# Optimization experiments

Hardware: AMD Instinct MI355X
Metric: run time of the kernel (lower is better)

## Reference

```python
import jax, jax.numpy as jnp
import numpy as np
from itertools import combinations

WAY = 5
TSS = 3  # temporal_set_size


def setup_inputs() -> dict:
    key = jax.random.key(0)
    k1, k2, k3 = jax.random.split(key, 3)
    n_support, n_queries, seq_len, D = 25, 400, 8, 2048
    d_out = D // 2
    support_set = jax.random.normal(k1, (n_support, seq_len, D), dtype=jnp.float32)
    queries = jax.random.normal(k2, (n_queries, seq_len, D), dtype=jnp.float32)
    support_labels = jnp.arange(n_support, dtype=jnp.int64) % WAY  # shot=5 per class
    W = jax.random.normal(k3, (d_out, TSS * D), dtype=jnp.float32) * 0.02
    b = jnp.zeros((d_out,), dtype=jnp.float32)
    return {"support_set": support_set, "support_labels": support_labels,
            "queries": queries, "W": W, "b": b}


def reference(support_set, support_labels, queries, W, b):
    # Dropout is identity at inference; omitted for determinism.
    n_s, seq_len, D = support_set.shape
    n_q = queries.shape[0]
    tup = jnp.asarray(list(combinations(range(seq_len), TSS)))  # [Tn, 3]
    Tn = tup.shape[0]
    # gather frame tuples and flatten: [N, Tn, 3*D]
    s = support_set[:, tup, :].reshape(n_s, Tn, TSS * D)
    q = queries[:, tup, :].reshape(n_q, Tn, TSS * D)
    # Linear + ReLU embedding
    qe = jax.nn.relu(q.reshape(n_q * Tn, TSS * D) @ W.T + b)          # [Q*Tn, d2]
    se = jax.nn.relu(s.reshape(n_s * Tn, TSS * D) @ W.T + b)
    se = se.reshape(n_s, Tn, -1)
    # group support by class (labels are static ints; shot per class is equal)
    order = jnp.argsort(support_labels, stable=True)                  # sorted by label
    cls_se = se[order.reshape(WAY, -1)].reshape(WAY, -1, se.shape[-1])  # [way, shot*Tn, d2]
    # pairwise Euclidean distances per class: ||q||^2 + ||s||^2 - 2 q.s
    q2 = jnp.sum(qe * qe, axis=-1)                                    # [Q*Tn]
    s2 = jnp.sum(cls_se * cls_se, axis=-1)                            # [way, shot*Tn]
    dots = jnp.einsum('qd,csd->cqs', qe, cls_se)                      # [way, Q*Tn, shot*Tn]
    dist = jnp.sqrt(jnp.maximum(q2[None, :, None] + s2[:, None, :] - 2.0 * dots, 0.0))
    min_dist = dist.min(axis=2).reshape(WAY, n_q, Tn)                 # min over class supports
    logits = -min_dist.mean(axis=2).T                                 # [n_q, way]
    return logits
```

## Files before the change

### kernel.cpp

```cpp
#include <hip/hip_runtime.h>
#include <math.h>

#define NSUP 25
#define NQ   400
#define SL   8
#define DIM  2048
#define DOUT 1024
#define WAY  5
#define TN   56
#define SHOT 5
#define QT   (NQ*TN)
#define STC  (SHOT*TN)
#define NFS  (NSUP*SL)
#define NFQ  (NQ*SL)
#define MF   (NFS+NFQ)
#define MFP  3584
#define PN   (3*DOUT)
#define NSE  1400
#define NSEP 1408

typedef __attribute__((ext_vector_type(8))) short short8;
typedef __attribute__((ext_vector_type(8))) int   int8v;
typedef __attribute__((ext_vector_type(4))) float f32x4;

#define GLOAD_LDS(g, l) __builtin_amdgcn_global_load_lds( \
    (const __attribute__((address_space(1))) unsigned*)(g), \
    (__attribute__((address_space(3))) unsigned*)(l), 16, 0, 0)

__device__ __forceinline__ unsigned short f2bf(float x) {
  unsigned u = __float_as_uint(x);
  u += 0x7fff + ((u >> 16) & 1);
  return (unsigned short)(u >> 16);
}
__device__ __forceinline__ float bf2f(unsigned short h) {
  return __uint_as_float(((unsigned)h) << 16);
}
__device__ __forceinline__ unsigned pk4_fp8(float a, float b, float c, float d) {
  unsigned p = __builtin_amdgcn_cvt_pk_fp8_f32(a, b, 0, false);
  p = __builtin_amdgcn_cvt_pk_fp8_f32(c, d, p, true);
  return p;
}
__device__ __forceinline__ float f8deq(unsigned b) {
  unsigned e = (b >> 3) & 15, m = b & 7;
  return e ? ldexpf((float)(8 + m), (int)e - 10) : ldexpf((float)m, -9);
}

__device__ __constant__ unsigned short TUP[TN] = {
  0x210,0x310,0x410,0x510,0x610,0x710,
  0x320,0x420,0x520,0x620,0x720,
  0x430,0x530,0x630,0x730,
  0x540,0x640,0x740,
  0x650,0x750,
  0x760,
  0x321,0x421,0x521,0x621,0x721,
  0x431,0x531,0x631,0x731,
  0x541,0x641,0x741,
  0x651,0x751,
  0x761,
  0x432,0x532,0x632,0x732,
  0x542,0x642,0x742,
  0x652,0x752,
  0x762,
  0x543,0x643,0x743,
  0x653,0x753,
  0x763,
  0x654,0x754,
  0x764,
  0x765
};

__global__ __launch_bounds__(256) void prep(
    const float* __restrict__ sup, const float* __restrict__ qry,
    const float* __restrict__ W,
    unsigned char* __restrict__ A8, unsigned char* __restrict__ W8,
    unsigned char* __restrict__ se8, float* __restrict__ s2,
    unsigned* __restrict__ pmin)
{
  int idx = blockIdx.x * 256 + threadIdx.x;
  {
    int e = idx * 4;
    int row = e >> 11, c = e & 2047;
    float4 v = make_float4(0.f, 0.f, 0.f, 0.f);
    if (row < NFS)      v = *(const float4*)(sup + (size_t)row * DIM + c);
    else if (row < MF)  v = *(const float4*)(qry + (size_t)(row - NFS) * DIM + c);
    *(unsigned*)(A8 + e) = pk4_fp8(v.x, v.y, v.z, v.w);
  }
  if (idx < PN*DIM/4) {
    int e = idx * 4;
    int n = e >> 11, c = e & 2047;
    const float4 v = *(const float4*)(W + (size_t)(n & 1023) * (3*DIM) + (n >> 10) * DIM + c);
    *(unsigned*)(W8 + e) = pk4_fp8(v.x*64.f, v.y*64.f, v.z*64.f, v.w*64.f);
  }
  if (idx < WAY * QT) pmin[idx] = 0x7F800000u;
  if (idx < (NSEP - NSE) * DOUT) se8[(size_t)NSE * DOUT + idx] = 0;
  if (idx < NSEP - NSE) s2[NSE + idx] = 0.f;
}

__device__ __forceinline__ void mfma_kloop_f8(
    const unsigned char* __restrict__ gA, const unsigned char* __restrict__ gB,
    int sa, int sb, int rowA0, int rowB0, int clampA,
    unsigned char* As, unsigned char* Bs,
    int w, int l, int nk, f32x4 acc[8][4])
{
  const int lrow = l >> 3;
  const int cswz = ((((l >> 1) & 3) ^ (lrow & 3)) * 2 + (l & 1)) * 16;
  unsigned offA[8], offB[4];
#pragma unroll
  for (int q = 0; q < 8; ++q)
    offA[q] = (unsigned)min(rowA0 + w*64 + q*8 + lrow, clampA) * sa + cswz;
#pragma unroll
  for (int q = 0; q < 4; ++q)
    offB[q] = (unsigned)(rowB0 + w*32 + q*8 + lrow) * sb + cswz;
  unsigned char* lA = As + (w*64) * 128;
  unsigned char* lB = Bs + (w*32) * 128;
  const int lane15 = l & 15, quad = l >> 4;
  const int wm = (w & 1) * 128, wn = (w >> 1) * 64;
  const int slot = (quad ^ (lane15 & 3)) * 32;

  int koff = 0;
  for (int kk = 0; kk < nk; ++kk, koff += 128) {
    __syncthreads();
#pragma unroll
    for (int q = 0; q < 8; ++q) GLOAD_LDS(gA + offA[q] + koff, lA + q*1024);
#pragma unroll
    for (int q = 0; q < 4; ++q) GLOAD_LDS(gB + offB[q] + koff, lB + q*1024);
    __syncthreads();
    int8v af[8];
#pragma unroll
    for (int i = 0; i < 8; ++i)
      af[i] = *(const int8v*)(As + (wm + i*16 + lane15)*128 + slot);
#pragma unroll
    for (int j = 0; j < 4; ++j) {
      int8v bf = *(const int8v*)(Bs + (wn + j*16 + lane15)*128 + slot);
#pragma unroll
      for (int i = 0; i < 8; ++i)
        acc[i][j] = __builtin_amdgcn_mfma_scale_f32_16x16x128_f8f6f4(
            af[i], bf, acc[i][j], 0, 0, 0, 0x7f7f7f7f, 0, 0x7f7f7f7f);
    }
  }
}

__global__ __launch_bounds__(256, 2) void gemm_embed_f8(
    const unsigned char* __restrict__ A8, const unsigned char* __restrict__ W8,
    unsigned short* __restrict__ P)
{
  __shared__ unsigned char As[256*128];
  __shared__ unsigned char Bs[128*128];
  const int bm = blockIdx.x * 256, bn = blockIdx.y * 128;
  const int tid = threadIdx.x, w = tid >> 6, l = tid & 63;
  const int lane15 = l & 15, quad = l >> 4;
  const int wm = (w & 1) * 128, wn = (w >> 1) * 64;

  f32x4 acc[8][4] = {};
  mfma_kloop_f8(A8, W8, DIM, DIM, bm, bn, MFP-1, As, Bs, w, l, DIM/128, acc);

#pragma unroll
  for (int i = 0; i < 8; ++i) {
#pragma unroll
    for (int r = 0; r < 4; ++r) {
      int row = bm + wm + i*16 + quad*4 + r;
      if (row < MF) {
#pragma unroll
        for (int j = 0; j < 4; ++j) {
          int col = bn + wn + j*16 + lane15;
          P[(size_t)row * PN + col] = f2bf(acc[i][j][r] * 0.015625f);
        }
      }
    }
  }
}

__global__ __launch_bounds__(256) void assemble_seq(
    const unsigned short* __restrict__ P, const float* __restrict__ bias,
    unsigned char* __restrict__ qe8, float* __restrict__ q2,
    unsigned char* __restrict__ se8, float* __restrict__ s2)
{
  __shared__ unsigned short sP[SL * PN];
  const int b2 = blockIdx.x, b = b2 >> 1, half = b2 & 1;
  const int tid = threadIdx.x, w = tid >> 6, l = tid & 63;

  const size_t base = (size_t)b * SL * PN;
#pragma unroll
  for (int qi = 0; qi < 12; ++qi) {
    int off = (qi * 256 + tid) * 8;
    *(short8*)&sP[off] = *(const short8*)(P + base + off);
  }
  __syncthreads();

  float4 bbv[4];
#pragma unroll
  for (int c = 0; c < 4; ++c)
    bbv[c] = *(const float4*)&bias[l*4 + c*256];

  const bool is_sup = b < NSUP;
  unsigned char* E = is_sup ? se8 : qe8;
  float* nrm = is_sup ? s2 : q2;
  int row_base;
  if (is_sup) { int cc = b % WAY, kk = b / WAY; row_base = cc * STC + kk * TN; }
  else        { row_base = (b - NSUP) * TN; }

  const int t_end = half * 28 + 28;
  for (int t = half * 28 + w; t < t_end; t += 4) {
    unsigned int tp = TUP[t];
    int f0 = tp & 15, f1 = (tp >> 4) & 15, f2 = (tp >> 8) & 15;
    int row = row_base + t;
    float ssq = 0.f;
#pragma unroll
    for (int c = 0; c < 4; ++c) {
      int o = l*4 + c*256;
      ushort4 a = *(const ushort4*)&sP[f0*PN + o];
      ushort4 bq = *(const ushort4*)&sP[f1*PN + DOUT + o];
      ushort4 d = *(const ushort4*)&sP[f2*PN + 2*DOUT + o];
      float z0 = fmaxf(bf2f(a.x) + bf2f(bq.x) + bf2f(d.x) + bbv[c].x, 0.f);
      float z1 = fmaxf(bf2f(a.y) + bf2f(bq.y) + bf2f(d.y) + bbv[c].y, 0.f);
      float z2 = fmaxf(bf2f(a.z) + bf2f(bq.z) + bf2f(d.z) + bbv[c].z, 0.f);
      float z3 = fmaxf(bf2f(a.w) + bf2f(bq.w) + bf2f(d.w) + bbv[c].w, 0.f);
      unsigned pk = pk4_fp8(z0, z1, z2, z3);
      *(unsigned*)&E[(size_t)row * DOUT + o] = pk;
      float x0 = f8deq(pk & 255),         x1 = f8deq((pk >> 8) & 255);
      float x2 = f8deq((pk >> 16) & 255), x3 = f8deq(pk >> 24);
      ssq += x0*x0 + x1*x1 + x2*x2 + x3*x3;
    }
#pragma unroll
    for (int off = 1; off < 64; off <<= 1) ssq += __shfl_xor(ssq, off, 64);
    if (l == 0) nrm[row] = ssq;
  }
}

__global__ __launch_bounds__(256, 2) void gemm_dist_f8(
    const unsigned char* __restrict__ qe8, const unsigned char* __restrict__ se8,
    const float* __restrict__ q2, const float* __restrict__ s2,
    unsigned* __restrict__ pmin)
{
  __shared__ unsigned char As[256*128];
  __shared__ unsigned char Bs[128*128];
  const int bm = blockIdx.x * 256;
  const int bn = blockIdx.y * 128;
  const int tid = threadIdx.x, w = tid >> 6, l = tid & 63;
  const int lane15 = l & 15, quad = l >> 4;
  const int wm = (w & 1) * 128, wn = (w >> 1) * 64;

  f32x4 acc[8][4] = {};
  mfma_kloop_f8(se8, qe8, DOUT, DOUT, bm, bn, NSEP-1, As, Bs, w, l, DOUT/128, acc);

  float s2v[8][4]; int clsv[8][4];
#pragma unroll
  for (int i = 0; i < 8; ++i)
#pragma unroll
    for (int r = 0; r < 4; ++r) {
      int sec = bm + wm + i*16 + quad*4 + r;
      s2v[i][r] = s2[min(sec, NSEP-1)];
      clsv[i][r] = sec / STC;
    }
#pragma unroll
  for (int i = 0; i < 8; ++i)
#pragma unroll
    for (int j = 0; j < 4; ++j)
#pragma unroll
      for (int r = 0; r < 4; ++r)
        acc[i][j][r] = fmaf(-2.f, acc[i][j][r], s2v[i][r]);

  float q2v[4];
#pragma unroll
  for (int j = 0; j < 4; ++j)
    q2v[j] = q2[bn + wn + j*16 + lane15];

  const int c_lo = (bm + wm) / STC;
  const int c_hi = min((bm + wm + 127) / STC, WAY - 1);
  for (int c = c_lo; c <= c_hi; ++c) {
#pragma unroll
    for (int j = 0; j < 4; ++j) {
      float mv = INFINITY;
#pragma unroll
      for (int i = 0; i < 8; ++i)
#pragma unroll
        for (int r = 0; r < 4; ++r)
          mv = fminf(mv, (clsv[i][r] == c) ? acc[i][j][r] : INFINITY);
      mv = fminf(mv, __shfl_xor(mv, 16, 64));
      mv = fminf(mv, __shfl_xor(mv, 32, 64));
      if (quad == 0) {
        float val = fmaxf(q2v[j] + mv, 0.f);
        atomicMin(&pmin[(size_t)c * QT + bn + wn + j*16 + lane15],
                  __float_as_uint(val));
      }
    }
  }
}

__global__ void finalize(const unsigned* __restrict__ pmin, float* __restrict__ out)
{
  int idx = blockIdx.x * blockDim.x + threadIdx.x;
  if (idx >= NQ * WAY) return;
  int i = idx / WAY, c = idx % WAY;
  float sum = 0.f;
  for (int t = 0; t < TN; ++t) {
    float v = __uint_as_float(pmin[(size_t)c * QT + i * TN + t]);
    sum += sqrtf(v);
  }
  out[i * WAY + c] = -sum * (1.f / (float)TN);
}

extern "C" void kernel_launch(void* const* d_in, const int* in_sizes, int n_in,
                              void* d_out, int out_size, void* d_ws, size_t ws_size,
                              hipStream_t stream) {
  const float* support = (const float*)d_in[0];
  const float* queries  = (const float*)d_in[2];
  const float* W        = (const float*)d_in[3];
  const float* bias     = (const float*)d_in[4];
  float* out = (float*)d_out;

  char* ws = (char*)d_ws;
  unsigned char* A8 = (unsigned char*)ws;           ws += (size_t)MFP * DIM;
  unsigned char* W8 = (unsigned char*)ws;           ws += (size_t)PN * DIM;
  unsigned short* P = (unsigned short*)ws;          ws += (size_t)MF * PN * 2;
  unsigned char* qe8 = (unsigned char*)ws;          ws += (size_t)QT * DOUT;
  unsigned char* se8 = (unsigned char*)ws;          ws += (size_t)NSEP * DOUT;
  float*         q2  = (float*)ws;                  ws += (size_t)QT * 4;
  float*         s2  = (float*)ws;                  ws += (size_t)NSEP * 4;
  unsigned*      pm  = (unsigned*)ws;

  prep<<<MFP*DIM/4/256, 256, 0, stream>>>(support, queries, W, A8, W8, se8, s2, pm);
  gemm_embed_f8<<<dim3(MFP/256, PN/128), 256, 0, stream>>>(A8, W8, P);
  assemble_seq<<<2*(NSUP + NQ), 256, 0, stream>>>(P, bias, qe8, q2, se8, s2);
  gemm_dist_f8<<<dim3(6, QT/128), 256, 0, stream>>>(qe8, se8, q2, s2, pm);
  finalize<<<(NQ*WAY + 255)/256, 256, 0, stream>>>(pm, out);
}
```

Baseline: 204.7 us.

## Rearrange LDS tile layout for MFMA fragments and swizzle dist-GEMM block order

Changes how the global-to-LDS async loads place data so each 16-row MFMA fragment is contiguous in LDS. Each lane now reads two 16-byte chunks 256 bytes apart instead of one 32-byte swizzled slot, which is meant to cut LDS bank conflicts on fragment reads. Separately, the distance GEMM launch becomes a 1D grid of 1050 blocks remapped so groups of 8 query tiles sweep all 6 support tiles together, aiming to improve L2 reuse of the query embeddings. The new mapping drops the XOR swizzle on the write side, which may add conflicts during the LDS fill.

```diff
diff --git a/kernel.cpp b/kernel.cpp
--- a/kernel.cpp
+++ b/kernel.cpp
@@ -21,6 +21,7 @@
 
 typedef __attribute__((ext_vector_type(8))) short short8;
 typedef __attribute__((ext_vector_type(8))) int   int8v;
+typedef __attribute__((ext_vector_type(4))) int   i4v;
 typedef __attribute__((ext_vector_type(4))) float f32x4;
 
 #define GLOAD_LDS(g, l) __builtin_amdgcn_global_load_lds( \
@@ -102,20 +103,25 @@
     unsigned char* As, unsigned char* Bs,
     int w, int l, int nk, f32x4 acc[8][4])
 {
-  const int lrow = l >> 3;
-  const int cswz = ((((l >> 1) & 3) ^ (lrow & 3)) * 2 + (l & 1)) * 16;
+  const int rl = l & 15, cl = l >> 4;
   unsigned offA[8], offB[4];
 #pragma unroll
-  for (int q = 0; q < 8; ++q)
-    offA[q] = (unsigned)min(rowA0 + w*64 + q*8 + lrow, clampA) * sa + cswz;
-#pragma unroll
-  for (int q = 0; q < 4; ++q)
-    offB[q] = (unsigned)(rowB0 + w*32 + q*8 + lrow) * sb + cswz;
+  for (int q = 0; q < 8; ++q) {
+    int row = rowA0 + w*64 + (q >> 1)*16 + rl;
+    int c   = (q*4 + cl) & 7;
+    offA[q] = (unsigned)min(row, clampA) * sa + c*16;
+  }
+#pragma unroll
+  for (int q = 0; q < 4; ++q) {
+    int row = rowB0 + w*32 + (q >> 1)*16 + rl;
+    int c   = (q*4 + cl) & 7;
+    offB[q] = (unsigned)row * sb + c*16;
+  }
   unsigned char* lA = As + (w*64) * 128;
   unsigned char* lB = Bs + (w*32) * 128;
   const int lane15 = l & 15, quad = l >> 4;
   const int wm = (w & 1) * 128, wn = (w >> 1) * 64;
-  const int slot = (quad ^ (lane15 & 3)) * 32;
+  const int off_lane = quad*512 + lane15*16;
 
   int koff = 0;
   for (int kk = 0; kk < nk; ++kk, koff += 128) {
@@ -127,11 +133,18 @@
     __syncthreads();
     int8v af[8];
 #pragma unroll
-    for (int i = 0; i < 8; ++i)
-      af[i] = *(const int8v*)(As + (wm + i*16 + lane15)*128 + slot);
+    for (int i = 0; i < 8; ++i) {
+      const unsigned char* ra = As + ((wm >> 4) + i)*2048 + off_lane;
+      i4v lo = *(const i4v*)(ra);
+      i4v hi = *(const i4v*)(ra + 256);
+      af[i] = __builtin_shufflevector(lo, hi, 0, 1, 2, 3, 4, 5, 6, 7);
+    }
 #pragma unroll
     for (int j = 0; j < 4; ++j) {
-      int8v bf = *(const int8v*)(Bs + (wn + j*16 + lane15)*128 + slot);
+      const unsigned char* rb = Bs + ((wn >> 4) + j)*2048 + off_lane;
+      i4v lo = *(const i4v*)(rb);
+      i4v hi = *(const i4v*)(rb + 256);
+      int8v bf = __builtin_shufflevector(lo, hi, 0, 1, 2, 3, 4, 5, 6, 7);
 #pragma unroll
       for (int i = 0; i < 8; ++i)
         acc[i][j] = __builtin_amdgcn_mfma_scale_f32_16x16x128_f8f6f4(
@@ -234,8 +247,12 @@
 {
   __shared__ unsigned char As[256*128];
   __shared__ unsigned char Bs[128*128];
-  const int bm = blockIdx.x * 256;
-  const int bn = blockIdx.y * 128;
+  int n = blockIdx.x;
+  int x, y;
+  if (n < 1008) { int g = n / 48, j = n % 48; y = g*8 + (j & 7); x = j >> 3; }
+  else          { int m = n - 1008; y = 168 + m % 7; x = m / 7; }
+  const int bm = x * 256;
+  const int bn = y * 128;
   const int tid = threadIdx.x, w = tid >> 6, l = tid & 63;
   const int lane15 = l & 15, quad = l >> 4;
   const int wm = (w & 1) * 128, wn = (w >> 1) * 64;
@@ -322,6 +339,6 @@
   prep<<<MFP*DIM/4/256, 256, 0, stream>>>(support, queries, W, A8, W8, se8, s2, pm);
   gemm_embed_f8<<<dim3(MFP/256, PN/128), 256, 0, stream>>>(A8, W8, P);
   assemble_seq<<<2*(NSUP + NQ), 256, 0, stream>>>(P, bias, qe8, q2, se8, s2);
-  gemm_dist_f8<<<dim3(6, QT/128), 256, 0, stream>>>(qe8, se8, q2, s2, pm);
+  gemm_dist_f8<<<1050, 256, 0, stream>>>(qe8, se8, q2, s2, pm);
   finalize<<<(NQ*WAY + 255)/256, 256, 0, stream>>>(pm, out);
 }
```

Measured after the change: 242.1 us. 1.18x slower.
